# Kernel tuning notes

Hardware: AMD Instinct MI355X
Metric: run time of the kernel (lower is better)

## Reference

```python
import jax, jax.numpy as jnp
import numpy as np

N_NODES = 100000
N_EDGES = 1600000
NODE_DIM = 128
EDGE_DIM = 48
GLOBAL_DIM = 64
N_GRAPHS = 64
HIDDEN = 256


def setup_inputs() -> dict:
    key = jax.random.key(0)
    ks = jax.random.split(key, 9)
    nodes = jax.random.normal(ks[0], (N_NODES, NODE_DIM), dtype=jnp.float32)
    edges = jax.random.normal(ks[1], (N_EDGES, EDGE_DIM), dtype=jnp.float32)
    edge_index = jax.random.randint(ks[2], (2, N_EDGES), 0, N_NODES, dtype=jnp.int64)
    batch = jnp.sort(jax.random.randint(ks[3], (N_NODES,), 0, N_GRAPHS, dtype=jnp.int64))
    graph_globals = jax.random.normal(ks[4], (N_GRAPHS, GLOBAL_DIM), dtype=jnp.float32)
    in_dim = NODE_DIM + EDGE_DIM + GLOBAL_DIM
    s1 = 1.0 / np.sqrt(in_dim)
    s2 = 1.0 / np.sqrt(HIDDEN)
    W1 = jax.random.uniform(ks[5], (in_dim, HIDDEN), minval=-s1, maxval=s1, dtype=jnp.float32)
    b1 = jax.random.uniform(ks[6], (HIDDEN,), minval=-s1, maxval=s1, dtype=jnp.float32)
    W2 = jax.random.uniform(ks[7], (HIDDEN, NODE_DIM), minval=-s2, maxval=s2, dtype=jnp.float32)
    b2 = jax.random.uniform(ks[8], (NODE_DIM,), minval=-s2, maxval=s2, dtype=jnp.float32)
    return {"nodes": nodes, "edges": edges, "edge_index": edge_index, "batch": batch,
            "graph_globals": graph_globals, "W1": W1, "b1": b1, "W2": W2, "b2": b2}


def reference(nodes, edges, edge_index, batch, graph_globals, W1, b1, W2, b2):
    recv = edge_index[1]
    # scatter-add edge messages to receiving nodes: [N, edge_dim]
    agg = jax.ops.segment_sum(edges, recv, num_segments=N_NODES)
    # gather per-graph globals to nodes: [N, global_dim]
    u = graph_globals[batch]
    x = jnp.concatenate([nodes, agg, u], axis=1)  # [N, node+edge+global]
    h = jax.nn.relu(x @ W1 + b1)
    return h @ W2 + b2  # new node features [N, node_dim]
```

## Files before the change

kernel.cpp:

```cpp
#include <hip/hip_runtime.h>
#include <hip/hip_bf16.h>
#include <stdint.h>

#define N_NODES   100000
#define N_EDGES   1600000
#define NODE_DIM  128
#define EDGE_DIM  48
#define GLOBAL_DIM 64
#define HIDDEN    256
#define KDIM      256
#define OUT_DIM   128

#define N_PAD     100352
#define SCAN_BLKS 98

#define AGG_OFF   0
#define AGG_BYTES (N_NODES * EDGE_DIM * 4)
#define W1P_OFF   (AGG_OFF + AGG_BYTES)
#define W1P_BYTES (KDIM * HIDDEN * 2)
#define W2P_OFF   (W1P_OFF + W1P_BYTES)
#define W2P_BYTES (HIDDEN * OUT_DIM * 2)
#define CNT_OFF   (W2P_OFF + W2P_BYTES)
#define CNT_BYTES (N_PAD * 4)
#define OFF_OFF   (CNT_OFF + CNT_BYTES)
#define CUR_OFF   (OFF_OFF + CNT_BYTES)
#define BSUM_OFF  (CUR_OFF + CNT_BYTES)
#define BSUM_BYTES 512
#define BEX_OFF   (BSUM_OFF + BSUM_BYTES)
#define EIDS_OFF  (BEX_OFF + BSUM_BYTES)

typedef short  short4_t  __attribute__((ext_vector_type(4)));
typedef short  short8_t  __attribute__((ext_vector_type(8)));
typedef float  floatx4   __attribute__((ext_vector_type(4)));

__device__ __forceinline__ short f2bf(float f) {
    union { float f; uint32_t u; } x; x.f = f;
    uint32_t r = (x.u + 0x7FFFu + ((x.u >> 16) & 1u)) >> 16;
    return (short)r;
}

__global__ void pack_w1(const float* __restrict__ W1, short* __restrict__ dst) {
    int tid = blockIdx.x * 256 + threadIdx.x;
    int k = tid >> 8, n = tid & 255;
    float v = (k < 240) ? W1[k * 256 + n] : 0.0f;
    int kg = k >> 5, kr = k & 31, quad = kr >> 3, j = kr & 7;
    int nt = n >> 4, nl = n & 15, lane = (quad << 4) | nl;
    dst[(((kg * 16 + nt) * 64) + lane) * 8 + j] = f2bf(v);
}

__global__ void pack_w2(const float* __restrict__ W2, short* __restrict__ dst) {
    int tid = blockIdx.x * 256 + threadIdx.x;
    int k = tid >> 7, n = tid & 127;
    float v = W2[k * 128 + n];
    int kg = k >> 5, kr = k & 31, quad = kr >> 3, j = kr & 7;
    int nt = n >> 4, nl = n & 15, lane = (quad << 4) | nl;
    dst[(((kg * 8 + nt) * 64) + lane) * 8 + j] = f2bf(v);
}

__global__ void count_kernel(const int* __restrict__ recv, int* __restrict__ cnt) {
    int e = blockIdx.x * 256 + threadIdx.x;
    if (e < N_EDGES) atomicAdd(&cnt[recv[e]], 1);
}

__global__ void scan_bsum(const int4* __restrict__ cnt4, int* __restrict__ bsum) {
    int4 v = cnt4[blockIdx.x * 256 + threadIdx.x];
    int s = v.x + v.y + v.z + v.w;
    #pragma unroll
    for (int d = 32; d; d >>= 1) s += __shfl_down(s, d);
    __shared__ int ws[4];
    if ((threadIdx.x & 63) == 0) ws[threadIdx.x >> 6] = s;
    __syncthreads();
    if (threadIdx.x == 0) bsum[blockIdx.x] = ws[0] + ws[1] + ws[2] + ws[3];
}

__global__ void scan_top(const int* __restrict__ bsum, int* __restrict__ bex) {
    __shared__ int tmp[128];
    int t = threadIdx.x;
    int v = (t < SCAN_BLKS) ? bsum[t] : 0;
    tmp[t] = v;
    __syncthreads();
    #pragma unroll
    for (int d = 1; d < 128; d <<= 1) {
        int add = (t >= d) ? tmp[t - d] : 0;
        __syncthreads();
        tmp[t] += add;
        __syncthreads();
    }
    if (t < SCAN_BLKS) bex[t] = tmp[t] - v;
}

__global__ void scan_write(const int4* __restrict__ cnt4, const int* __restrict__ bex,
                           int4* __restrict__ off4, int4* __restrict__ cur4) {
    int t = threadIdx.x, b = blockIdx.x;
    int4 v = cnt4[b * 256 + t];
    int tsum = v.x + v.y + v.z + v.w;
    int lane = t & 63, w = t >> 6;
    int x = tsum;
    #pragma unroll
    for (int d = 1; d < 64; d <<= 1) {
        int y = __shfl_up(x, d);
        if (lane >= d) x += y;
    }
    __shared__ int wsum[4];
    if (lane == 63) wsum[w] = x;
    __syncthreads();
    int wb = 0;
    if (w > 0) wb += wsum[0];
    if (w > 1) wb += wsum[1];
    if (w > 2) wb += wsum[2];
    int base = bex[b] + wb + (x - tsum);
    int4 o;
    o.x = base;
    o.y = base + v.x;
    o.z = base + v.x + v.y;
    o.w = base + v.x + v.y + v.z;
    off4[b * 256 + t] = o;
    cur4[b * 256 + t] = o;
}

__global__ void fill_kernel(const int* __restrict__ recv, int* __restrict__ cur,
                            int* __restrict__ eids) {
    int e = blockIdx.x * 256 + threadIdx.x;
    if (e < N_EDGES) {
        int pos = atomicAdd(&cur[recv[e]], 1);
        eids[pos] = e;
    }
}

__global__ __launch_bounds__(256)
void gather_kernel(const float* __restrict__ edges, const int* __restrict__ eids,
                   const int* __restrict__ off, const int* __restrict__ cnt,
                   float* __restrict__ agg) {
    int node = blockIdx.x * 4 + (threadIdx.x >> 6);
    int lane = threadIdx.x & 63;
    if (node >= N_NODES) return;
    int o = off[node], c = cnt[node];
    float acc = 0.0f;
    int i = 0;
    for (; i + 4 <= c; i += 4) {
        int e0 = eids[o + i + 0];
        int e1 = eids[o + i + 1];
        int e2 = eids[o + i + 2];
        int e3 = eids[o + i + 3];
        if (lane < 48) {
            float v0 = edges[(size_t)e0 * 48 + lane];
            float v1 = edges[(size_t)e1 * 48 + lane];
            float v2 = edges[(size_t)e2 * 48 + lane];
            float v3 = edges[(size_t)e3 * 48 + lane];
            acc += (v0 + v1) + (v2 + v3);
        }
    }
    for (; i < c; ++i) {
        int e = eids[o + i];
        if (lane < 48) acc += edges[(size_t)e * 48 + lane];
    }
    if (lane < 48) agg[(size_t)node * 48 + lane] = acc;
}

#define LDS_W 264
__global__ __launch_bounds__(256, 2)
void mlp_kernel(const float* __restrict__ nodes,
                const float* __restrict__ agg,
                const int* __restrict__ batch,
                const float* __restrict__ gg,
                const short8_t* __restrict__ w1p,
                const short8_t* __restrict__ w2p,
                const float* __restrict__ b1,
                const float* __restrict__ b2,
                float* __restrict__ out) {
    __shared__ short xt[64 * LDS_W];

    const int t = threadIdx.x;
    const int m0 = blockIdx.x * 64;

    const float4* nodes4 = (const float4*)nodes;
    const float4* agg4   = (const float4*)agg;
    const float4* gg4    = (const float4*)gg;

    #pragma unroll
    for (int i = 0; i < 8; ++i) {
        int f = t + 256 * i;
        int r = f >> 5, c4 = f & 31;
        int node = m0 + r;
        float4 v = make_float4(0.f, 0.f, 0.f, 0.f);
        if (node < N_NODES) v = nodes4[node * 32 + c4];
        short4_t s; s.x = f2bf(v.x); s.y = f2bf(v.y); s.z = f2bf(v.z); s.w = f2bf(v.w);
        *(short4_t*)(&xt[r * LDS_W + c4 * 4]) = s;
    }
    #pragma unroll
    for (int i = 0; i < 3; ++i) {
        int f = t + 256 * i;
        int r = f / 12, c4 = f - r * 12;
        int node = m0 + r;
        float4 v = make_float4(0.f, 0.f, 0.f, 0.f);
        if (node < N_NODES) v = agg4[node * 12 + c4];
        short4_t s; s.x = f2bf(v.x); s.y = f2bf(v.y); s.z = f2bf(v.z); s.w = f2bf(v.w);
        *(short4_t*)(&xt[r * LDS_W + (32 + c4) * 4]) = s;
    }
    #pragma unroll
    for (int i = 0; i < 4; ++i) {
        int f = t + 256 * i;
        int r = f >> 4, c4 = f & 15;
        int node = m0 + r;
        float4 v = make_float4(0.f, 0.f, 0.f, 0.f);
        if (node < N_NODES) { int g = batch[node]; v = gg4[g * 16 + c4]; }
        short4_t s; s.x = f2bf(v.x); s.y = f2bf(v.y); s.z = f2bf(v.z); s.w = f2bf(v.w);
        *(short4_t*)(&xt[r * LDS_W + (44 + c4) * 4]) = s;
    }
    {
        int r = t >> 2, c4 = t & 3;
        short4_t s; s.x = 0; s.y = 0; s.z = 0; s.w = 0;
        *(short4_t*)(&xt[r * LDS_W + (60 + c4) * 4]) = s;
    }
    __syncthreads();

    const int w    = t >> 6;
    const int lane = t & 63;
    const int q    = lane >> 4;
    const int ln   = lane & 15;

    floatx4 acc[4][4];
    #pragma unroll
    for (int a = 0; a < 4; ++a)
        #pragma unroll
        for (int b = 0; b < 4; ++b) acc[a][b] = 0.0f;

    #pragma unroll
    for (int kg = 0; kg < 8; ++kg) {
        short8_t A[4], B[4];
        #pragma unroll
        for (int mt = 0; mt < 4; ++mt)
            A[mt] = *(const short8_t*)(&xt[(mt * 16 + ln) * LDS_W + kg * 32 + q * 8]);
        #pragma unroll
        for (int ntl = 0; ntl < 4; ++ntl) {
            int nt = w * 4 + ntl;
            B[ntl] = (const short8_t&)w1p[(kg * 16 + nt) * 64 + lane];
        }
        #pragma unroll
        for (int mt = 0; mt < 4; ++mt)
            #pragma unroll
            for (int ntl = 0; ntl < 4; ++ntl)
                acc[mt][ntl] = __builtin_amdgcn_mfma_f32_16x16x32_bf16(
                    A[mt], B[ntl], acc[mt][ntl], 0, 0, 0);
    }

    float b1v[4];
    #pragma unroll
    for (int ntl = 0; ntl < 4; ++ntl) b1v[ntl] = b1[w * 64 + ntl * 16 + ln];

    __syncthreads();

    #pragma unroll
    for (int mt = 0; mt < 4; ++mt)
        #pragma unroll
        for (int ntl = 0; ntl < 4; ++ntl)
            #pragma unroll
            for (int r = 0; r < 4; ++r) {
                float v = acc[mt][ntl][r] + b1v[ntl];
                v = fmaxf(v, 0.0f);
                xt[(mt * 16 + q * 4 + r) * LDS_W + w * 64 + ntl * 16 + ln] = f2bf(v);
            }
    __syncthreads();

    floatx4 acc2[4][2];
    #pragma unroll
    for (int a = 0; a < 4; ++a)
        #pragma unroll
        for (int b = 0; b < 2; ++b) acc2[a][b] = 0.0f;

    #pragma unroll
    for (int kg = 0; kg < 8; ++kg) {
        short8_t A[4], B[2];
        #pragma unroll
        for (int mt = 0; mt < 4; ++mt)
            A[mt] = *(const short8_t*)(&xt[(mt * 16 + ln) * LDS_W + kg * 32 + q * 8]);
        #pragma unroll
        for (int ntl = 0; ntl < 2; ++ntl) {
            int nt = w * 2 + ntl;
            B[ntl] = (const short8_t&)w2p[(kg * 8 + nt) * 64 + lane];
        }
        #pragma unroll
        for (int mt = 0; mt < 4; ++mt)
            #pragma unroll
            for (int ntl = 0; ntl < 2; ++ntl)
                acc2[mt][ntl] = __builtin_amdgcn_mfma_f32_16x16x32_bf16(
                    A[mt], B[ntl], acc2[mt][ntl], 0, 0, 0);
    }

    float b2v[2];
    #pragma unroll
    for (int ntl = 0; ntl < 2; ++ntl) b2v[ntl] = b2[w * 32 + ntl * 16 + ln];

    #pragma unroll
    for (int mt = 0; mt < 4; ++mt)
        #pragma unroll
        for (int ntl = 0; ntl < 2; ++ntl)
            #pragma unroll
            for (int r = 0; r < 4; ++r) {
                int node = m0 + mt * 16 + q * 4 + r;
                if (node < N_NODES)
                    out[node * 128 + w * 32 + ntl * 16 + ln] = acc2[mt][ntl][r] + b2v[ntl];
            }
}

extern "C" void kernel_launch(void* const* d_in, const int* in_sizes, int n_in,
                              void* d_out, int out_size, void* d_ws, size_t ws_size,
                              hipStream_t stream) {
    const float* nodes = (const float*)d_in[0];
    const float* edges = (const float*)d_in[1];
    const int* edge_index = (const int*)d_in[2];
    const int* batch = (const int*)d_in[3];
    const float* gg = (const float*)d_in[4];
    const float* W1 = (const float*)d_in[5];
    const float* b1 = (const float*)d_in[6];
    const float* W2 = (const float*)d_in[7];
    const float* b2 = (const float*)d_in[8];
    float* out = (float*)d_out;

    char* ws = (char*)d_ws;
    float* agg  = (float*)(ws + AGG_OFF);
    short* w1p  = (short*)(ws + W1P_OFF);
    short* w2p  = (short*)(ws + W2P_OFF);
    int*   cnt  = (int*)  (ws + CNT_OFF);
    int*   off  = (int*)  (ws + OFF_OFF);
    int*   cur  = (int*)  (ws + CUR_OFF);
    int*   bsum = (int*)  (ws + BSUM_OFF);
    int*   bex  = (int*)  (ws + BEX_OFF);
    int*   eids = (int*)  (ws + EIDS_OFF);
    const int* recv = edge_index + N_EDGES;

    hipMemsetAsync(cnt, 0, CNT_BYTES, stream);
    pack_w1<<<256, 256, 0, stream>>>(W1, w1p);
    pack_w2<<<128, 256, 0, stream>>>(W2, w2p);
    count_kernel<<<(N_EDGES + 255) / 256, 256, 0, stream>>>(recv, cnt);
    scan_bsum<<<SCAN_BLKS, 256, 0, stream>>>((const int4*)cnt, bsum);
    scan_top<<<1, 128, 0, stream>>>(bsum, bex);
    scan_write<<<SCAN_BLKS, 256, 0, stream>>>((const int4*)cnt, bex, (int4*)off, (int4*)cur);
    fill_kernel<<<(N_EDGES + 255) / 256, 256, 0, stream>>>(recv, cur, eids);
    gather_kernel<<<(N_NODES + 3) / 4, 256, 0, stream>>>(edges, eids, off, cnt, agg);
    mlp_kernel<<<(N_NODES + 63) / 64, 256, 0, stream>>>(
        nodes, agg, batch, gg,
        (const short8_t*)w1p, (const short8_t*)w2p, b1, b2, out);
}
```

Measured before the change: 762.9 us.

## Fuse edge gather into MLP kernel and make CSR fill atomic-free via ranks

The count kernel now stores each edge's atomic return value as its rank within the receiving node. The fill kernel then places edge ids at off[recv]+rank with no atomics, and the cursor array disappears. The separate gather kernel is removed: the MLP kernel sums edge features for its 64 nodes directly into the shared-memory tile, so the fp32 agg buffer is never written to or read back from global memory. Both edge-index kernels now read recv as int4. The cost is that the latency-bound gather now runs inside a kernel limited to about two blocks per CU, with wave-wide loops bounded by the largest degree in the wave, which may hide memory latency worse than the old standalone gather did.

```diff
diff --git a/kernel.cpp b/kernel.cpp
--- a/kernel.cpp
+++ b/kernel.cpp
@@ -14,20 +14,19 @@
 #define N_PAD     100352
 #define SCAN_BLKS 98
 
-#define AGG_OFF   0
-#define AGG_BYTES (N_NODES * EDGE_DIM * 4)
-#define W1P_OFF   (AGG_OFF + AGG_BYTES)
+#define W1P_OFF   0
 #define W1P_BYTES (KDIM * HIDDEN * 2)
 #define W2P_OFF   (W1P_OFF + W1P_BYTES)
 #define W2P_BYTES (HIDDEN * OUT_DIM * 2)
 #define CNT_OFF   (W2P_OFF + W2P_BYTES)
 #define CNT_BYTES (N_PAD * 4)
 #define OFF_OFF   (CNT_OFF + CNT_BYTES)
-#define CUR_OFF   (OFF_OFF + CNT_BYTES)
-#define BSUM_OFF  (CUR_OFF + CNT_BYTES)
+#define BSUM_OFF  (OFF_OFF + CNT_BYTES)
 #define BSUM_BYTES 512
 #define BEX_OFF   (BSUM_OFF + BSUM_BYTES)
-#define EIDS_OFF  (BEX_OFF + BSUM_BYTES)
+#define RANK_OFF  (BEX_OFF + BSUM_BYTES)
+#define RANK_BYTES (N_EDGES * 4)
+#define EIDS_OFF  (RANK_OFF + RANK_BYTES)
 
 typedef short  short4_t  __attribute__((ext_vector_type(4)));
 typedef short  short8_t  __attribute__((ext_vector_type(8)));
@@ -57,9 +56,17 @@
     dst[(((kg * 8 + nt) * 64) + lane) * 8 + j] = f2bf(v);
 }
 
-__global__ void count_kernel(const int* __restrict__ recv, int* __restrict__ cnt) {
-    int e = blockIdx.x * 256 + threadIdx.x;
-    if (e < N_EDGES) atomicAdd(&cnt[recv[e]], 1);
+__global__ void count_kernel(const int4* __restrict__ recv4, int* __restrict__ cnt,
+                             int4* __restrict__ rank4) {
+    int tid = blockIdx.x * 256 + threadIdx.x;
+    if (tid >= N_EDGES / 4) return;
+    int4 r = recv4[tid];
+    int4 k;
+    k.x = atomicAdd(&cnt[r.x], 1);
+    k.y = atomicAdd(&cnt[r.y], 1);
+    k.z = atomicAdd(&cnt[r.z], 1);
+    k.w = atomicAdd(&cnt[r.w], 1);
+    rank4[tid] = k;
 }
 
 __global__ void scan_bsum(const int4* __restrict__ cnt4, int* __restrict__ bsum) {
@@ -90,7 +97,7 @@
 }
 
 __global__ void scan_write(const int4* __restrict__ cnt4, const int* __restrict__ bex,
-                           int4* __restrict__ off4, int4* __restrict__ cur4) {
+                           int4* __restrict__ off4) {
     int t = threadIdx.x, b = blockIdx.x;
     int4 v = cnt4[b * 256 + t];
     int tsum = v.x + v.y + v.z + v.w;
@@ -115,52 +122,27 @@
     o.z = base + v.x + v.y;
     o.w = base + v.x + v.y + v.z;
     off4[b * 256 + t] = o;
-    cur4[b * 256 + t] = o;
-}
-
-__global__ void fill_kernel(const int* __restrict__ recv, int* __restrict__ cur,
-                            int* __restrict__ eids) {
-    int e = blockIdx.x * 256 + threadIdx.x;
-    if (e < N_EDGES) {
-        int pos = atomicAdd(&cur[recv[e]], 1);
-        eids[pos] = e;
-    }
-}
-
-__global__ __launch_bounds__(256)
-void gather_kernel(const float* __restrict__ edges, const int* __restrict__ eids,
-                   const int* __restrict__ off, const int* __restrict__ cnt,
-                   float* __restrict__ agg) {
-    int node = blockIdx.x * 4 + (threadIdx.x >> 6);
-    int lane = threadIdx.x & 63;
-    if (node >= N_NODES) return;
-    int o = off[node], c = cnt[node];
-    float acc = 0.0f;
-    int i = 0;
-    for (; i + 4 <= c; i += 4) {
-        int e0 = eids[o + i + 0];
-        int e1 = eids[o + i + 1];
-        int e2 = eids[o + i + 2];
-        int e3 = eids[o + i + 3];
-        if (lane < 48) {
-            float v0 = edges[(size_t)e0 * 48 + lane];
-            float v1 = edges[(size_t)e1 * 48 + lane];
-            float v2 = edges[(size_t)e2 * 48 + lane];
-            float v3 = edges[(size_t)e3 * 48 + lane];
-            acc += (v0 + v1) + (v2 + v3);
-        }
-    }
-    for (; i < c; ++i) {
-        int e = eids[o + i];
-        if (lane < 48) acc += edges[(size_t)e * 48 + lane];
-    }
-    if (lane < 48) agg[(size_t)node * 48 + lane] = acc;
+}
+
+__global__ void fill_kernel(const int4* __restrict__ recv4, const int4* __restrict__ rank4,
+                            const int* __restrict__ off, int* __restrict__ eids) {
+    int tid = blockIdx.x * 256 + threadIdx.x;
+    if (tid >= N_EDGES / 4) return;
+    int4 r = recv4[tid];
+    int4 k = rank4[tid];
+    int e = tid * 4;
+    eids[off[r.x] + k.x] = e + 0;
+    eids[off[r.y] + k.y] = e + 1;
+    eids[off[r.z] + k.z] = e + 2;
+    eids[off[r.w] + k.w] = e + 3;
 }
 
 #define LDS_W 264
 __global__ __launch_bounds__(256, 2)
 void mlp_kernel(const float* __restrict__ nodes,
-                const float* __restrict__ agg,
+                const int* __restrict__ eids,
+                const int* __restrict__ off,
+                const float4* __restrict__ edges4,
                 const int* __restrict__ batch,
                 const float* __restrict__ gg,
                 const short8_t* __restrict__ w1p,
@@ -172,9 +154,56 @@
 
     const int t = threadIdx.x;
     const int m0 = blockIdx.x * 64;
+    const int w    = t >> 6;
+    const int lane = t & 63;
+
+    {
+        int sub = lane / 12;
+        int c4g = lane - sub * 12;
+        bool gact = lane < 48;
+        #pragma unroll
+        for (int qi = 0; qi < 4; ++qi) {
+            int r = w * 16 + qi * 4 + sub;
+            int node = m0 + r;
+            int o = 0, c = 0;
+            if (gact && node < N_NODES) {
+                o = off[node];
+                c = off[node + 1] - o;
+            }
+            int cmax = c;
+            #pragma unroll
+            for (int d = 1; d < 64; d <<= 1) cmax = max(cmax, __shfl_xor(cmax, d));
+            float4 acc = make_float4(0.f, 0.f, 0.f, 0.f);
+            int i = 0;
+            for (; i + 2 <= cmax; i += 2) {
+                float4 v0 = make_float4(0.f, 0.f, 0.f, 0.f);
+                float4 v1 = make_float4(0.f, 0.f, 0.f, 0.f);
+                if (i < c) {
+                    int e0 = eids[o + i];
+                    v0 = edges4[(size_t)e0 * 12 + c4g];
+                }
+                if (i + 1 < c) {
+                    int e1 = eids[o + i + 1];
+                    v1 = edges4[(size_t)e1 * 12 + c4g];
+                }
+                acc.x += v0.x + v1.x; acc.y += v0.y + v1.y;
+                acc.z += v0.z + v1.z; acc.w += v0.w + v1.w;
+            }
+            if (i < cmax && i < c) {
+                int e0 = eids[o + i];
+                float4 v0 = edges4[(size_t)e0 * 12 + c4g];
+                acc.x += v0.x; acc.y += v0.y; acc.z += v0.z; acc.w += v0.w;
+            }
+            if (gact) {
+                short4_t s;
+                s.x = f2bf(acc.x); s.y = f2bf(acc.y);
+                s.z = f2bf(acc.z); s.w = f2bf(acc.w);
+                *(short4_t*)(&xt[r * LDS_W + (32 + c4g) * 4]) = s;
+            }
+        }
+    }
 
     const float4* nodes4 = (const float4*)nodes;
-    const float4* agg4   = (const float4*)agg;
     const float4* gg4    = (const float4*)gg;
 
     #pragma unroll
@@ -188,16 +217,6 @@
         *(short4_t*)(&xt[r * LDS_W + c4 * 4]) = s;
     }
     #pragma unroll
-    for (int i = 0; i < 3; ++i) {
-        int f = t + 256 * i;
-        int r = f / 12, c4 = f - r * 12;
-        int node = m0 + r;
-        float4 v = make_float4(0.f, 0.f, 0.f, 0.f);
-        if (node < N_NODES) v = agg4[node * 12 + c4];
-        short4_t s; s.x = f2bf(v.x); s.y = f2bf(v.y); s.z = f2bf(v.z); s.w = f2bf(v.w);
-        *(short4_t*)(&xt[r * LDS_W + (32 + c4) * 4]) = s;
-    }
-    #pragma unroll
     for (int i = 0; i < 4; ++i) {
         int f = t + 256 * i;
         int r = f >> 4, c4 = f & 15;
@@ -214,10 +233,8 @@
     }
     __syncthreads();
 
-    const int w    = t >> 6;
-    const int lane = t & 63;
-    const int q    = lane >> 4;
-    const int ln   = lane & 15;
+    const int q  = lane >> 4;
+    const int ln = lane & 15;
 
     floatx4 acc[4][4];
     #pragma unroll
@@ -318,27 +335,27 @@
     float* out = (float*)d_out;
 
     char* ws = (char*)d_ws;
-    float* agg  = (float*)(ws + AGG_OFF);
     short* w1p  = (short*)(ws + W1P_OFF);
     short* w2p  = (short*)(ws + W2P_OFF);
     int*   cnt  = (int*)  (ws + CNT_OFF);
     int*   off  = (int*)  (ws + OFF_OFF);
-    int*   cur  = (int*)  (ws + CUR_OFF);
     int*   bsum = (int*)  (ws + BSUM_OFF);
     int*   bex  = (int*)  (ws + BEX_OFF);
+    int*   rank = (int*)  (ws + RANK_OFF);
     int*   eids = (int*)  (ws + EIDS_OFF);
     const int* recv = edge_index + N_EDGES;
 
     hipMemsetAsync(cnt, 0, CNT_BYTES, stream);
     pack_w1<<<256, 256, 0, stream>>>(W1, w1p);
     pack_w2<<<128, 256, 0, stream>>>(W2, w2p);
-    count_kernel<<<(N_EDGES + 255) / 256, 256, 0, stream>>>(recv, cnt);
+    count_kernel<<<(N_EDGES / 4 + 255) / 256, 256, 0, stream>>>(
+        (const int4*)recv, cnt, (int4*)rank);
     scan_bsum<<<SCAN_BLKS, 256, 0, stream>>>((const int4*)cnt, bsum);
     scan_top<<<1, 128, 0, stream>>>(bsum, bex);
-    scan_write<<<SCAN_BLKS, 256, 0, stream>>>((const int4*)cnt, bex, (int4*)off, (int4*)cur);
-    fill_kernel<<<(N_EDGES + 255) / 256, 256, 0, stream>>>(recv, cur, eids);
-    gather_kernel<<<(N_NODES + 3) / 4, 256, 0, stream>>>(edges, eids, off, cnt, agg);
+    scan_write<<<SCAN_BLKS, 256, 0, stream>>>((const int4*)cnt, bex, (int4*)off);
+    fill_kernel<<<(N_EDGES / 4 + 255) / 256, 256, 0, stream>>>(
+        (const int4*)recv, (const int4*)rank, off, eids);
     mlp_kernel<<<(N_NODES + 63) / 64, 256, 0, stream>>>(
-        nodes, agg, batch, gg,
+        nodes, eids, off, (const float4*)edges, batch, gg,
         (const short8_t*)w1p, (const short8_t*)w2p, b1, b2, out);
 }
```

Measured after the change: 742.6 us. 1.03x faster.
